# Kernel optimization log

Measured on AMD Instinct MI355X. Metric: run time of the kernel, lower is better.

Reference implementation:

```python
import jax, jax.numpy as jnp
import numpy as np

TEMP = 0.05
EPS = 1e-12


def setup_inputs() -> dict:
    key = jax.random.key(0)
    k1, k2, k3, k4 = jax.random.split(key, 4)
    B, D, N = 2048, 128, 100000
    inputs = jax.random.normal(k1, (B, D), dtype=jnp.float32)
    indexes = jax.random.randint(k2, (B,), 0, N, dtype=jnp.int64)
    labels = jax.random.randint(k3, (N,), 0, N, dtype=jnp.int64)
    feats = jax.random.normal(k4, (N, D), dtype=jnp.float32)
    # memory bank rows are kept L2-normalized by the module's update logic
    features = feats / jnp.linalg.norm(feats, axis=1, keepdims=True)
    return {"inputs": inputs, "indexes": indexes, "labels": labels, "features": features}


def reference(inputs, indexes, labels, features):
    # F.normalize(inputs, dim=1)
    inputs_n = inputs / jnp.maximum(jnp.linalg.norm(inputs, axis=1, keepdims=True), EPS)
    # targets = labels[indexes]
    targets = labels[indexes]
    # logits = inputs_n @ features.T / temp  -> [B, N]
    logits = jnp.matmul(inputs_n, features.T) / TEMP
    # cross-entropy with mean reduction
    logz = jax.nn.logsumexp(logits, axis=1)
    picked = jnp.take_along_axis(logits, targets[:, None], axis=1)[:, 0]
    loss = jnp.mean(logz - picked)
    return loss
```

## Files before the change

kernel.cpp:

```cpp
#include <hip/hip_runtime.h>

typedef float f32x4 __attribute__((ext_vector_type(4)));
typedef int   int4v __attribute__((ext_vector_type(4)));
typedef int   int8v __attribute__((ext_vector_type(8)));

#define AS1 __attribute__((address_space(1)))
#define AS3 __attribute__((address_space(3)))

#define NROWS 2048
#define NCOLS 100000
#define NPAD  100352
#define NCHUNK 98
#define K2C  28.853900817779268f
#define PADC 7.2552607e-7f
#define SCLA 0x7F7F7F7Fu
#define SCLB 0x7C7C7C7Cu

__global__ void k_prep(const float* __restrict__ X, const int* __restrict__ idx,
                       const int* __restrict__ lab, const float* __restrict__ F,
                       unsigned short* __restrict__ A8, float* __restrict__ picked) {
  int wid = threadIdx.x >> 6, lane = threadIdx.x & 63;
  int row = blockIdx.x * 4 + wid;
  int t = lab[idx[row]];
  float2 v = ((const float2*)(X + (size_t)row * 128))[lane];
  float2 f = ((const float2*)(F + (size_t)t * 128))[lane];
  float ss = v.x * v.x + v.y * v.y;
  float dp = v.x * f.x + v.y * f.y;
#pragma unroll
  for (int m = 1; m < 64; m <<= 1) {
    ss += __shfl_xor(ss, m, 64);
    dp += __shfl_xor(dp, m, 64);
  }
  float invn = 1.0f / fmaxf(sqrtf(ss), 1e-12f);
  float s = invn * K2C;
  int w = __builtin_amdgcn_cvt_pk_fp8_f32(v.x * s, v.y * s, 0, false);
  A8[row * 64 + lane] = (unsigned short)(w & 0xFFFF);
  if (lane == 0) picked[row] = 20.0f * dp * invn;
}

__global__ void k_conv(const float* __restrict__ F, unsigned char* __restrict__ Fq) {
  const int NG8 = NPAD * 16;
  const int NV8 = NCOLS * 16;
  int stride = gridDim.x * blockDim.x;
  for (int g = blockIdx.x * blockDim.x + threadIdx.x; g < NG8; g += stride) {
    float4 a = make_float4(0.f, 0.f, 0.f, 0.f), b = a;
    if (g < NV8) {
      a = ((const float4*)F)[2 * g];
      b = ((const float4*)F)[2 * g + 1];
    }
    int w0 = __builtin_amdgcn_cvt_pk_fp8_f32(a.x * 8.f, a.y * 8.f, 0, false);
    w0 = __builtin_amdgcn_cvt_pk_fp8_f32(a.z * 8.f, a.w * 8.f, w0, true);
    int w1 = __builtin_amdgcn_cvt_pk_fp8_f32(b.x * 8.f, b.y * 8.f, 0, false);
    w1 = __builtin_amdgcn_cvt_pk_fp8_f32(b.z * 8.f, b.w * 8.f, w1, true);
    ((int2*)Fq)[g] = make_int2(w0, w1);
  }
}

__global__ __launch_bounds__(256, 2) void k_gemm(
    const unsigned short* __restrict__ A8,
    const unsigned char* __restrict__ Fq,
    float* __restrict__ part) {
  __shared__ unsigned char ring[3][64 * 128];
  __shared__ float xpose[4][64];
  const int tid = threadIdx.x;
  const int wid = tid >> 6, lane = tid & 63;
  const int lrow = lane & 15, lk = lane >> 4;

  const int slot = blockIdx.x >> 3;
  const int xcd  = blockIdx.x & 7;
  const int mtile = slot & 7;
  const int chunk = (slot >> 3) * 8 + xcd;
  if (chunk >= NCHUNK) return;
  const int row0 = mtile * 256 + wid * 64;

  const unsigned char* A8b = (const unsigned char*)A8;
  int8v af[4];
#pragma unroll
  for (int mf = 0; mf < 4; ++mf) {
    const unsigned char* ap = A8b + (size_t)(row0 + mf * 16 + lrow) * 128 + lk * 32;
    int4v lo = *(const int4v*)ap;
    int4v hi = *(const int4v*)(ap + 16);
    af[mf][0] = lo[0]; af[mf][1] = lo[1]; af[mf][2] = lo[2]; af[mf][3] = lo[3];
    af[mf][4] = hi[0]; af[mf][5] = hi[1]; af[mf][6] = hi[2]; af[mf][7] = hi[3];
  }

  float racc[4][4];
#pragma unroll
  for (int mf = 0; mf < 4; ++mf)
#pragma unroll
    for (int j = 0; j < 4; ++j) racc[mf][j] = 0.f;

  const int nbase = chunk * 1024;

  auto issue1 = [&](unsigned char* dst, int h, int it) {
    int off16 = it * 256 + tid;
    int col = off16 >> 3, up = off16 & 7;
    int ul = up ^ (col & 7);
    const unsigned char* src = Fq + (size_t)(nbase + h * 64 + col) * 128 + ul * 16;
    __builtin_amdgcn_global_load_lds((const AS1 void*)src,
                                     (AS3 void*)(dst + off16 * 16), 16, 0, 0);
  };

  auto half_body = [&](const unsigned char* sb, unsigned char* stDst, int hst) {
#pragma unroll
    for (int j = 0; j < 4; ++j) {
      int c = j * 16 + lrow;
      const unsigned char* cb = sb + c * 128;
      int x = c & 7;
      int4v lo = *(const int4v*)(cb + (((lk * 2)     ^ x) * 16));
      int4v hi = *(const int4v*)(cb + (((lk * 2 + 1) ^ x) * 16));
      int8v b8;
      b8[0] = lo[0]; b8[1] = lo[1]; b8[2] = lo[2]; b8[3] = lo[3];
      b8[4] = hi[0]; b8[5] = hi[1]; b8[6] = hi[2]; b8[7] = hi[3];
      if (stDst && (j & 1) == 0) issue1(stDst, hst, j >> 1);
      f32x4 acc[4];
#pragma unroll
      for (int mf = 0; mf < 4; ++mf)
        acc[mf] = (f32x4){-K2C, -K2C, -K2C, -K2C};
      __builtin_amdgcn_s_setprio(1);
#pragma unroll
      for (int mf = 0; mf < 4; ++mf)
        acc[mf] = __builtin_amdgcn_mfma_scale_f32_16x16x128_f8f6f4(
            af[mf], b8, acc[mf], 0, 0, 0, SCLA, 0, SCLB);
      __builtin_amdgcn_s_setprio(0);
#pragma unroll
      for (int mf = 0; mf < 4; ++mf)
#pragma unroll
        for (int jj = 0; jj < 4; ++jj)
          racc[mf][jj] += __builtin_amdgcn_exp2f(acc[mf][jj]);
    }
  };

#pragma unroll
  for (int h = 0; h < 2; ++h)
#pragma unroll
    for (int it = 0; it < 2; ++it) issue1(&ring[h][0], h, it);

  int rs = 0;
#pragma unroll 1
  for (int h = 0; h < 14; ++h) {
    asm volatile("s_waitcnt vmcnt(2)" ::: "memory");
    __builtin_amdgcn_s_barrier();
    int ss = rs + 2 - (rs >= 1 ? 3 : 0);
    half_body(&ring[rs][0], &ring[ss][0], h + 2);
    rs = (rs == 2) ? 0 : rs + 1;
  }
  asm volatile("s_waitcnt vmcnt(2)" ::: "memory");
  __builtin_amdgcn_s_barrier();
  half_body(&ring[rs][0], nullptr, 0);
  rs = (rs == 2) ? 0 : rs + 1;
  asm volatile("s_waitcnt vmcnt(0)" ::: "memory");
  __builtin_amdgcn_s_barrier();
  half_body(&ring[rs][0], nullptr, 0);

#pragma unroll
  for (int mf = 0; mf < 4; ++mf)
#pragma unroll
    for (int j = 0; j < 4; ++j) {
      float v = racc[mf][j];
      v += __shfl_xor(v, 1, 64);
      v += __shfl_xor(v, 2, 64);
      v += __shfl_xor(v, 4, 64);
      v += __shfl_xor(v, 8, 64);
      if (lrow == 0) xpose[wid][mf * 16 + lk * 4 + j] = v;
    }
  __syncthreads();
  part[(size_t)chunk * NROWS + row0 + lane] = xpose[wid][lane];
}

__global__ void k_loss1(const float* __restrict__ part, float* __restrict__ psum) {
  int rb = blockIdx.x & 7, cb = blockIdx.x >> 3;
  int b = rb * 256 + threadIdx.x;
  float s = 0.f;
#pragma unroll
  for (int k = 0; k < 14; ++k)
    s += part[(size_t)(cb * 14 + k) * NROWS + b];
  psum[(size_t)cb * NROWS + b] = s;
}

__global__ void k_final(const float* __restrict__ psum, const float* __restrict__ picked,
                        float* __restrict__ out) {
  int tid = threadIdx.x;
  float lb = 0.f;
#pragma unroll
  for (int rr = 0; rr < 2; ++rr) {
    int b = rr * 1024 + tid;
    float tot = 0.f;
#pragma unroll
    for (int cb = 0; cb < 7; ++cb) tot += psum[(size_t)cb * NROWS + b];
    tot -= PADC;
    lb += 20.0f + logf(tot) - picked[b];
  }
#pragma unroll
  for (int m = 1; m < 64; m <<= 1) lb += __shfl_xor(lb, m, 64);
  __shared__ float red[16];
  if ((tid & 63) == 0) red[tid >> 6] = lb;
  __syncthreads();
  if (tid == 0) {
    float s = 0.f;
#pragma unroll
    for (int i = 0; i < 16; ++i) s += red[i];
    out[0] = s * (1.0f / 2048.0f);
  }
}

extern "C" void kernel_launch(void* const* d_in, const int* in_sizes, int n_in,
                              void* d_out, int out_size, void* d_ws, size_t ws_size,
                              hipStream_t stream) {
  const float* inputs  = (const float*)d_in[0];
  const int*   indexes = (const int*)d_in[1];
  const int*   labels  = (const int*)d_in[2];
  const float* feats   = (const float*)d_in[3];
  float* out = (float*)d_out;

  char* ws = (char*)d_ws;
  unsigned short* A8 = (unsigned short*)(ws + 0);
  unsigned char*  Fq = (unsigned char*)(ws + 262144);
  float* part   = (float*)(ws + 13107200);
  float* psum   = (float*)(ws + 13910016);
  float* picked = (float*)(ws + 13967360);

  hipLaunchKernelGGL(k_prep,  dim3(512),  dim3(256),  0, stream, inputs, indexes, labels, feats, A8, picked);
  hipLaunchKernelGGL(k_conv,  dim3(2048), dim3(256),  0, stream, feats, Fq);
  hipLaunchKernelGGL(k_gemm,  dim3(832),  dim3(256),  0, stream, A8, Fq, part);
  hipLaunchKernelGGL(k_loss1, dim3(56),   dim3(256),  0, stream, part, psum);
  hipLaunchKernelGGL(k_final, dim3(1),    dim3(1024), 0, stream, psum, picked, out);
}
```

Before: 68.86 us.

## Fuse fp8 conversion of feature bank into GEMM kernel, drop separate conversion pass

Removes the standalone kernel that quantized the feature bank to fp8 in workspace. The GEMM kernel now loads fp32 feature rows into registers and converts them to fp8 itself. It writes the swizzled result into the LDS ring, zeroing out-of-range padding columns through a scale factor. This avoids a kernel launch and the fp8 write and re-read of the bank. The cost is four times more bytes fetched per tile and conversion repeated by each of the eight row tiles sharing a chunk. The async global-to-LDS prefetch is also replaced by register staging with a full vmcnt wait each step, which shortens load/compute overlap.

```diff
diff --git a/kernel.cpp b/kernel.cpp
--- a/kernel.cpp
+++ b/kernel.cpp
@@ -9,7 +9,6 @@
 
 #define NROWS 2048
 #define NCOLS 100000
-#define NPAD  100352
 #define NCHUNK 98
 #define K2C  28.853900817779268f
 #define PADC 7.2552607e-7f
@@ -38,27 +37,9 @@
   if (lane == 0) picked[row] = 20.0f * dp * invn;
 }
 
-__global__ void k_conv(const float* __restrict__ F, unsigned char* __restrict__ Fq) {
-  const int NG8 = NPAD * 16;
-  const int NV8 = NCOLS * 16;
-  int stride = gridDim.x * blockDim.x;
-  for (int g = blockIdx.x * blockDim.x + threadIdx.x; g < NG8; g += stride) {
-    float4 a = make_float4(0.f, 0.f, 0.f, 0.f), b = a;
-    if (g < NV8) {
-      a = ((const float4*)F)[2 * g];
-      b = ((const float4*)F)[2 * g + 1];
-    }
-    int w0 = __builtin_amdgcn_cvt_pk_fp8_f32(a.x * 8.f, a.y * 8.f, 0, false);
-    w0 = __builtin_amdgcn_cvt_pk_fp8_f32(a.z * 8.f, a.w * 8.f, w0, true);
-    int w1 = __builtin_amdgcn_cvt_pk_fp8_f32(b.x * 8.f, b.y * 8.f, 0, false);
-    w1 = __builtin_amdgcn_cvt_pk_fp8_f32(b.z * 8.f, b.w * 8.f, w1, true);
-    ((int2*)Fq)[g] = make_int2(w0, w1);
-  }
-}
-
 __global__ __launch_bounds__(256, 2) void k_gemm(
     const unsigned short* __restrict__ A8,
-    const unsigned char* __restrict__ Fq,
+    const float* __restrict__ F,
     float* __restrict__ part) {
   __shared__ unsigned char ring[3][64 * 128];
   __shared__ float xpose[4][64];
@@ -92,16 +73,51 @@
 
   const int nbase = chunk * 1024;
 
-  auto issue1 = [&](unsigned char* dst, int h, int it) {
-    int off16 = it * 256 + tid;
-    int col = off16 >> 3, up = off16 & 7;
-    int ul = up ^ (col & 7);
-    const unsigned char* src = Fq + (size_t)(nbase + h * 64 + col) * 128 + ul * 16;
-    __builtin_amdgcn_global_load_lds((const AS1 void*)src,
-                                     (AS3 void*)(dst + off16 * 16), 16, 0, 0);
+  int scol0, sul0, scol1, sul1;
+  {
+    int off16 = tid;
+    scol0 = off16 >> 3; sul0 = (off16 & 7) ^ (scol0 & 7);
+    off16 = 256 + tid;
+    scol1 = off16 >> 3; sul1 = (off16 & 7) ^ (scol1 & 7);
+  }
+
+  float4 sA0, sA1, sA2, sA3, sB0, sB1, sB2, sB3;
+  float sc0, sc1;
+
+  auto loadS = [&](int h) {
+    int g0 = nbase + h * 64 + scol0;
+    int g1 = nbase + h * 64 + scol1;
+    sc0 = (g0 < NCOLS) ? 8.0f : 0.0f;
+    sc1 = (g1 < NCOLS) ? 8.0f : 0.0f;
+    const float4* p0 = (const float4*)(F + (size_t)min(g0, NCOLS - 1) * 128 + sul0 * 16);
+    const float4* p1 = (const float4*)(F + (size_t)min(g1, NCOLS - 1) * 128 + sul1 * 16);
+    sA0 = p0[0]; sA1 = p0[1]; sA2 = p0[2]; sA3 = p0[3];
+    sB0 = p1[0]; sB1 = p1[1]; sB2 = p1[2]; sB3 = p1[3];
   };
 
-  auto half_body = [&](const unsigned char* sb, unsigned char* stDst, int hst) {
+  auto cvtWrite = [&](unsigned char* dst) {
+    int w0, w1, w2, w3;
+    w0 = __builtin_amdgcn_cvt_pk_fp8_f32(sA0.x * sc0, sA0.y * sc0, 0, false);
+    w0 = __builtin_amdgcn_cvt_pk_fp8_f32(sA0.z * sc0, sA0.w * sc0, w0, true);
+    w1 = __builtin_amdgcn_cvt_pk_fp8_f32(sA1.x * sc0, sA1.y * sc0, 0, false);
+    w1 = __builtin_amdgcn_cvt_pk_fp8_f32(sA1.z * sc0, sA1.w * sc0, w1, true);
+    w2 = __builtin_amdgcn_cvt_pk_fp8_f32(sA2.x * sc0, sA2.y * sc0, 0, false);
+    w2 = __builtin_amdgcn_cvt_pk_fp8_f32(sA2.z * sc0, sA2.w * sc0, w2, true);
+    w3 = __builtin_amdgcn_cvt_pk_fp8_f32(sA3.x * sc0, sA3.y * sc0, 0, false);
+    w3 = __builtin_amdgcn_cvt_pk_fp8_f32(sA3.z * sc0, sA3.w * sc0, w3, true);
+    *(int4v*)(dst + (tid) * 16) = (int4v){w0, w1, w2, w3};
+    w0 = __builtin_amdgcn_cvt_pk_fp8_f32(sB0.x * sc1, sB0.y * sc1, 0, false);
+    w0 = __builtin_amdgcn_cvt_pk_fp8_f32(sB0.z * sc1, sB0.w * sc1, w0, true);
+    w1 = __builtin_amdgcn_cvt_pk_fp8_f32(sB1.x * sc1, sB1.y * sc1, 0, false);
+    w1 = __builtin_amdgcn_cvt_pk_fp8_f32(sB1.z * sc1, sB1.w * sc1, w1, true);
+    w2 = __builtin_amdgcn_cvt_pk_fp8_f32(sB2.x * sc1, sB2.y * sc1, 0, false);
+    w2 = __builtin_amdgcn_cvt_pk_fp8_f32(sB2.z * sc1, sB2.w * sc1, w2, true);
+    w3 = __builtin_amdgcn_cvt_pk_fp8_f32(sB3.x * sc1, sB3.y * sc1, 0, false);
+    w3 = __builtin_amdgcn_cvt_pk_fp8_f32(sB3.z * sc1, sB3.w * sc1, w3, true);
+    *(int4v*)(dst + (256 + tid) * 16) = (int4v){w0, w1, w2, w3};
+  };
+
+  auto half_compute = [&](const unsigned char* sb) {
 #pragma unroll
     for (int j = 0; j < 4; ++j) {
       int c = j * 16 + lrow;
@@ -112,7 +128,6 @@
       int8v b8;
       b8[0] = lo[0]; b8[1] = lo[1]; b8[2] = lo[2]; b8[3] = lo[3];
       b8[4] = hi[0]; b8[5] = hi[1]; b8[6] = hi[2]; b8[7] = hi[3];
-      if (stDst && (j & 1) == 0) issue1(stDst, hst, j >> 1);
       f32x4 acc[4];
 #pragma unroll
       for (int mf = 0; mf < 4; ++mf)
@@ -131,27 +146,29 @@
     }
   };
 
-#pragma unroll
-  for (int h = 0; h < 2; ++h)
-#pragma unroll
-    for (int it = 0; it < 2; ++it) issue1(&ring[h][0], h, it);
+  loadS(0);
+  asm volatile("s_waitcnt vmcnt(0)" ::: "memory");
+  cvtWrite(&ring[0][0]);
+  loadS(1);
+  asm volatile("s_waitcnt vmcnt(0)" ::: "memory");
+  cvtWrite(&ring[1][0]);
+  __syncthreads();
 
   int rs = 0;
 #pragma unroll 1
   for (int h = 0; h < 14; ++h) {
-    asm volatile("s_waitcnt vmcnt(2)" ::: "memory");
+    loadS(h + 2);
+    half_compute(&ring[rs][0]);
+    asm volatile("s_waitcnt vmcnt(0)" ::: "memory");
+    int ws = rs + 2 - (rs >= 1 ? 3 : 0);
+    cvtWrite(&ring[ws][0]);
+    asm volatile("s_waitcnt lgkmcnt(0)" ::: "memory");
     __builtin_amdgcn_s_barrier();
-    int ss = rs + 2 - (rs >= 1 ? 3 : 0);
-    half_body(&ring[rs][0], &ring[ss][0], h + 2);
     rs = (rs == 2) ? 0 : rs + 1;
   }
-  asm volatile("s_waitcnt vmcnt(2)" ::: "memory");
-  __builtin_amdgcn_s_barrier();
-  half_body(&ring[rs][0], nullptr, 0);
+  half_compute(&ring[rs][0]);
   rs = (rs == 2) ? 0 : rs + 1;
-  asm volatile("s_waitcnt vmcnt(0)" ::: "memory");
-  __builtin_amdgcn_s_barrier();
-  half_body(&ring[rs][0], nullptr, 0);
+  half_compute(&ring[rs][0]);
 
 #pragma unroll
   for (int mf = 0; mf < 4; ++mf)
@@ -215,14 +232,12 @@
 
   char* ws = (char*)d_ws;
   unsigned short* A8 = (unsigned short*)(ws + 0);
-  unsigned char*  Fq = (unsigned char*)(ws + 262144);
-  float* part   = (float*)(ws + 13107200);
-  float* psum   = (float*)(ws + 13910016);
-  float* picked = (float*)(ws + 13967360);
+  float* part   = (float*)(ws + 262144);
+  float* psum   = (float*)(ws + 1064960);
+  float* picked = (float*)(ws + 1122304);
 
   hipLaunchKernelGGL(k_prep,  dim3(512),  dim3(256),  0, stream, inputs, indexes, labels, feats, A8, picked);
-  hipLaunchKernelGGL(k_conv,  dim3(2048), dim3(256),  0, stream, feats, Fq);
-  hipLaunchKernelGGL(k_gemm,  dim3(832),  dim3(256),  0, stream, A8, Fq, part);
+  hipLaunchKernelGGL(k_gemm,  dim3(832),  dim3(256),  0, stream, A8, feats, part);
   hipLaunchKernelGGL(k_loss1, dim3(56),   dim3(256),  0, stream, part, psum);
   hipLaunchKernelGGL(k_final, dim3(1),    dim3(1024), 0, stream, psum, picked, out);
 }
```

After: 69.88 us. About the same (+1.5%).
